# Optimization experiments

Hardware: AMD Instinct MI355X
Metric: run time of the kernel (lower is better)

Reference implementation:

```python
import jax, jax.numpy as jnp
from jax import lax
import numpy as np

T, B, D, H = 512, 256, 128, 256
SHIFT = 0.0


def setup_inputs() -> dict:
    key = jax.random.key(0)
    ks = jax.random.split(key, 11)
    s_in = 1.0 / np.sqrt(D + H)
    s_cl = 1.0 / np.sqrt(H)
    return {
        "inputs": jax.random.normal(ks[0], (T, B, D), dtype=jnp.float32),
        "Wf": jax.random.normal(ks[1], (H, D + H), dtype=jnp.float32) * s_in,
        "bf": jax.random.normal(ks[2], (H,), dtype=jnp.float32) * s_in,
        "Wi": jax.random.normal(ks[3], (H, D + H), dtype=jnp.float32) * s_in,
        "bi": jax.random.normal(ks[4], (H,), dtype=jnp.float32) * s_in,
        "Wg": jax.random.normal(ks[5], (H, D + H), dtype=jnp.float32) * s_in,
        "bg": jax.random.normal(ks[6], (H,), dtype=jnp.float32) * s_in,
        "Wo": jax.random.normal(ks[7], (H, D + H), dtype=jnp.float32) * s_in,
        "bo": jax.random.normal(ks[8], (H,), dtype=jnp.float32) * s_in,
        "Wc": jax.random.normal(ks[9], (1, H), dtype=jnp.float32) * s_cl,
        "bc": jax.random.normal(ks[10], (1,), dtype=jnp.float32) * s_cl,
    }


def reference(inputs, Wf, bf, Wi, bi, Wg, bg, Wo, bo, Wc, bc):
    # Fuse the four gate linears into one GEMM per step: [4H, D+H]
    W = jnp.concatenate([Wf, Wi, Wg, Wo], axis=0)
    b = jnp.concatenate([bf, bi, bg, bo], axis=0)
    h = W.shape[0] // 4
    batch = inputs.shape[1]

    def step(carry, x):
        hx, cx = carry
        combined = jnp.concatenate([x, hx], axis=1)      # [B, D+H]
        z = combined @ W.T + b                            # [B, 4H]
        f = jax.nn.sigmoid(z[:, 0 * h:1 * h])
        i = jax.nn.sigmoid(z[:, 1 * h:2 * h])
        g = jnp.tanh(z[:, 2 * h:3 * h])
        o = jax.nn.sigmoid(z[:, 3 * h:4 * h])
        cx = f * cx + i * g
        hx = o * jnp.tanh(cx)
        return (hx, cx), hx

    h0 = jnp.zeros((batch, h), dtype=inputs.dtype)
    c0 = jnp.zeros((batch, h), dtype=inputs.dtype)
    (hx, cx), hs = lax.scan(step, (h0, c0), inputs)       # hs: [T, B, H]

    logits = hs @ Wc.T + bc                               # [T, B, 1]
    probs = jax.nn.sigmoid(logits + SHIFT)
    return (jnp.concatenate([probs, 1.0 - probs], axis=-1), hx, cx)
```

## Files before the change

kernel.cpp:

```cpp
#include <hip/hip_runtime.h>
#include <hip/hip_bf16.h>


#define T_STEPS 512
#define BATCH   256
#define DIN     128
#define HID     256
#define KDIM    384
#define LDK     392
#define GRIDN   128
#define BLOCKT  512
#define NPOLL   96

typedef __attribute__((ext_vector_type(8))) short short8;
typedef __attribute__((ext_vector_type(4))) short short4v;
typedef __attribute__((ext_vector_type(4))) float f32x4;

__device__ __forceinline__ unsigned short f2bf(float f) {
    unsigned u = __float_as_uint(f);
    unsigned r = (u + 0x7FFFu + ((u >> 16) & 1u)) >> 16;
    return (unsigned short)r;
}
__device__ __forceinline__ float bf2f(unsigned short s) {
    return __uint_as_float(((unsigned)s) << 16);
}
__device__ __forceinline__ float sigmoid_f(float x) {
    return 1.f / (1.f + __expf(-x));
}
__device__ __forceinline__ float tanh_f(float x) {
    float e = __expf(2.f * x);
    return 1.f - 2.f / (e + 1.f);
}
__device__ __forceinline__ void poll_load2_sc0(const unsigned int* p, uint4& a,
                                               uint4& b) {
    asm volatile(
        "global_load_dwordx4 %0, %2, off sc0\n\t"
        "global_load_dwordx4 %1, %2, off offset:16 sc0\n\t"
        "s_waitcnt vmcnt(0)"
        : "=&v"(a), "=&v"(b) : "v"(p) : "memory");
}
__device__ __forceinline__ void poll_load2_sc1(const unsigned int* p, uint4& a,
                                               uint4& b) {
    asm volatile(
        "global_load_dwordx4 %0, %2, off sc1\n\t"
        "global_load_dwordx4 %1, %2, off offset:16 sc1\n\t"
        "s_waitcnt vmcnt(0)"
        : "=&v"(a), "=&v"(b) : "v"(p) : "memory");
}
__device__ __forceinline__ void store_plain_u32(unsigned int* p, unsigned int v) {
    asm volatile("global_store_dword %0, %1, off" :: "v"(p), "v"(v) : "memory");
}
__device__ __forceinline__ void store_sc1_u32(unsigned int* p, unsigned int v) {
    asm volatile("global_store_dword %0, %1, off sc1" :: "v"(p), "v"(v) : "memory");
}
__device__ __forceinline__ unsigned pack2bf(unsigned lo, unsigned hi) {
    return (hi & 0xFFFF0000u) | (lo >> 16);
}
__device__ __forceinline__ bool tags_ok2(const uint4& a, const uint4& b,
                                         unsigned tag) {
    return ((a.x ^ tag) & 0xFFFFu) == 0 && ((a.y ^ tag) & 0xFFFFu) == 0 &&
           ((a.z ^ tag) & 0xFFFFu) == 0 && ((a.w ^ tag) & 0xFFFFu) == 0 &&
           ((b.x ^ tag) & 0xFFFFu) == 0 && ((b.y ^ tag) & 0xFFFFu) == 0 &&
           ((b.z ^ tag) & 0xFFFFu) == 0 && ((b.w ^ tag) & 0xFFFFu) == 0;
}

__global__ __launch_bounds__(256) void pack_w(
    const float* __restrict__ Wf, const float* __restrict__ Wi,
    const float* __restrict__ Wg, const float* __restrict__ Wo,
    unsigned short* __restrict__ Wp) {
    int idx = blockIdx.x * 256 + threadIdx.x;
    int n = idx / KDIM;
    int k = idx - n * KDIM;
    int g = n >> 8, j = n & 255;
    const float* s = (g == 0) ? Wf : (g == 1) ? Wi : (g == 2) ? Wg : Wo;
    Wp[idx] = f2bf(s[j * KDIM + k]);
}

__global__ __launch_bounds__(256) void pack_b(
    const float* __restrict__ bf, const float* __restrict__ bi,
    const float* __restrict__ bg, const float* __restrict__ bo,
    float* __restrict__ bp) {
    int n = blockIdx.x * 256 + threadIdx.x;
    int g = n >> 8, j = n & 255;
    const float* s = (g == 0) ? bf : (g == 1) ? bi : (g == 2) ? bg : bo;
    bp[n] = s[j];
}

__global__ __launch_bounds__(256) void init_k(unsigned int* __restrict__ hxp) {
    int tid = blockIdx.x * 256 + threadIdx.x;
    hxp[tid] = 0u;
    hxp[65536 + tid] = 0u;
    hxp[131072 + tid] = 0u;
    hxp[196608 + tid] = 0u;
}

__global__ __launch_bounds__(BLOCKT, 1) void lstm_persist(
    const float* __restrict__ X,
    const unsigned short* __restrict__ W,
    const float* __restrict__ bias,
    unsigned int* __restrict__ hxp,
    unsigned short* __restrict__ hist,
    float* __restrict__ out) {
    __shared__ __align__(16) unsigned short W_s[128 * LDK];
    __shared__ __align__(16) unsigned short comb_s[16 * LDK];
    __shared__ __align__(16) float z_s[8 * 272];
    __shared__ int fastok_s;

    const int tid = threadIdx.x;
    const int bg = blockIdx.x & 15, jg = blockIdx.x >> 4;
    const int b0 = bg * 16, j0 = jg * 32;
    const int wave = tid >> 6, lane = tid & 63;
    const int l16 = lane & 15, quad = lane >> 4;
    const int bi = tid >> 5, jj = tid & 31;
    const int b = b0 + bi, j = j0 + jj;

#pragma unroll
    for (int c = 0; c < 12; ++c) {
        int q = c * 512 + tid;
        int row = q / 48, c8 = q - row * 48;
        int g = row >> 5, jr = row & 31;
        short8 v = *(const short8*)(W + ((g * 256 + j0 + jr) * KDIM + c8 * 8));
        *(short8*)(&W_s[row * LDK + c8 * 8]) = v;
    }
    const float bs0 = bias[0 * HID + j];
    const float bs1 = bias[1 * HID + j];
    const float bs2 = bias[2 * HID + j];
    const float bs3 = bias[3 * HID + j];
    if (tid == 0) fastok_s = 1;

    float c_reg = 0.f;
    float h_final = 0.f;

    const unsigned short* arow = &comb_s[l16 * LDK + quad * 8];
    const unsigned short* brow = &W_s[(wave * 16 + l16) * LDK + quad * 8];

    float4 xv = *(const float4*)(X + b * DIN + jj * 4);
    {
        short4v r;
        r.x = (short)f2bf(xv.x); r.y = (short)f2bf(xv.y);
        r.z = (short)f2bf(xv.z); r.w = (short)f2bf(xv.w);
        *(short4v*)(&comb_s[bi * LDK + jj * 4]) = r;
    }
    xv = *(const float4*)(X + (size_t)1 * BATCH * DIN + b * DIN + jj * 4);
    __syncthreads();

    f32x4 acc_x0 = {0.f, 0.f, 0.f, 0.f}, acc_x1 = {0.f, 0.f, 0.f, 0.f};
#pragma unroll
    for (int kt = 0; kt < 2; ++kt) {
        short8 a0 = *(const short8*)(arow + (2 * kt) * 32);
        short8 b0v = *(const short8*)(brow + (2 * kt) * 32);
        short8 a1 = *(const short8*)(arow + (2 * kt + 1) * 32);
        short8 b1v = *(const short8*)(brow + (2 * kt + 1) * 32);
        acc_x0 = __builtin_amdgcn_mfma_f32_16x16x32_bf16(a0, b0v, acc_x0, 0, 0, 0);
        acc_x1 = __builtin_amdgcn_mfma_f32_16x16x32_bf16(a1, b1v, acc_x1, 0, 0, 0);
    }

    for (int k = 0; k < T_STEPS; ++k) {
        const unsigned tag = (unsigned)k;
        const unsigned int* fb =
            hxp + (k & 1) * 65536 + (b0 + bi) * HID + jj * 8;
        const unsigned int* sb = fb + 131072;
        uint4 a, bq;
        const int usefast = fastok_s;

        if (usefast) {
            int tries = NPOLL;
            bool ok = false;
            for (;;) {
                poll_load2_sc0(fb, a, bq);
                if (tags_ok2(a, bq, tag)) { ok = true; break; }
                if (--tries == 0) break;
                __builtin_amdgcn_s_sleep(1);
            }
            if (!ok) {
                fastok_s = 0;
                for (;;) {
                    poll_load2_sc1(sb, a, bq);
                    if (tags_ok2(a, bq, tag)) break;
                    __builtin_amdgcn_s_sleep(1);
                }
            }
        } else {
            for (;;) {
                poll_load2_sc1(sb, a, bq);
                if (tags_ok2(a, bq, tag)) break;
                __builtin_amdgcn_s_sleep(1);
            }
        }

        {
            uint4 p0;
            p0.x = pack2bf(a.x, a.y);   p0.y = pack2bf(a.z, a.w);
            p0.z = pack2bf(bq.x, bq.y); p0.w = pack2bf(bq.z, bq.w);
            *(uint4*)(&comb_s[bi * LDK + DIN + jj * 8]) = p0;
        }
        __syncthreads();

        f32x4 acc0 = acc_x0, acc1 = acc_x1;
#pragma unroll
        for (int kt = 2; kt < 6; ++kt) {
            short8 a0 = *(const short8*)(arow + (2 * kt) * 32);
            short8 b0v = *(const short8*)(brow + (2 * kt) * 32);
            short8 a1 = *(const short8*)(arow + (2 * kt + 1) * 32);
            short8 b1v = *(const short8*)(brow + (2 * kt + 1) * 32);
            acc0 = __builtin_amdgcn_mfma_f32_16x16x32_bf16(a0, b0v, acc0, 0, 0, 0);
            acc1 = __builtin_amdgcn_mfma_f32_16x16x32_bf16(a1, b1v, acc1, 0, 0, 0);
        }
#pragma unroll
        for (int r = 0; r < 4; ++r)
            z_s[wave * 272 + (quad * 4 + r) * 17 + l16] = acc0[r] + acc1[r];
        __syncthreads();

        const int zc = bi * 17 + (jj & 15);
        const int zw = (jj >> 4) * 272;
        float zf = z_s[zw + 0 * 544 + zc] + bs0;
        float zi = z_s[zw + 1 * 544 + zc] + bs1;
        float zg = z_s[zw + 2 * 544 + zc] + bs2;
        float zo = z_s[zw + 3 * 544 + zc] + bs3;
        float fg = sigmoid_f(zf);
        float ig = sigmoid_f(zi);
        float gg = tanh_f(zg);
        float og = sigmoid_f(zo);
        c_reg = fg * c_reg + ig * gg;
        float hval = og * tanh_f(c_reg);
        unsigned short hb = f2bf(hval);
        unsigned int hword = ((unsigned)hb << 16) | (unsigned)(k + 1);
        unsigned int* fdst = hxp + ((k + 1) & 1) * 65536 + b * HID + j;
        store_plain_u32(fdst, hword);
        store_sc1_u32(fdst + 131072, hword);
        hist[(size_t)k * BATCH * HID + b * HID + j] = hb;

        if (k + 1 < T_STEPS) {
            short4v r;
            r.x = (short)f2bf(xv.x); r.y = (short)f2bf(xv.y);
            r.z = (short)f2bf(xv.z); r.w = (short)f2bf(xv.w);
            *(short4v*)(&comb_s[bi * LDK + jj * 4]) = r;
            if (k + 2 < T_STEPS) {
                xv = *(const float4*)(X + (size_t)(k + 2) * BATCH * DIN +
                                      b * DIN + jj * 4);
            }
        } else {
            h_final = hval;
        }
        __syncthreads();

        if (k + 1 < T_STEPS) {
            f32x4 ax0 = {0.f, 0.f, 0.f, 0.f}, ax1 = {0.f, 0.f, 0.f, 0.f};
#pragma unroll
            for (int kt = 0; kt < 2; ++kt) {
                short8 a0 = *(const short8*)(arow + (2 * kt) * 32);
                short8 b0v = *(const short8*)(brow + (2 * kt) * 32);
                short8 a1 = *(const short8*)(arow + (2 * kt + 1) * 32);
                short8 b1v = *(const short8*)(brow + (2 * kt + 1) * 32);
                ax0 = __builtin_amdgcn_mfma_f32_16x16x32_bf16(a0, b0v, ax0, 0, 0, 0);
                ax1 = __builtin_amdgcn_mfma_f32_16x16x32_bf16(a1, b1v, ax1, 0, 0, 0);
            }
            acc_x0 = ax0; acc_x1 = ax1;
        }
    }

    out[T_STEPS * BATCH * 2 + b * HID + j] = h_final;
    out[T_STEPS * BATCH * 2 + BATCH * HID + b * HID + j] = c_reg;
}

__global__ __launch_bounds__(256) void probs_k(
    const unsigned short* __restrict__ hist, const float* __restrict__ Wc,
    const float* __restrict__ bc, float* __restrict__ out) {
    const int wave = threadIdx.x >> 6, lane = threadIdx.x & 63;
    const size_t row = (size_t)blockIdx.x * 4 + wave;
    const unsigned short* h = hist + row * HID;
    short4v hv = *(const short4v*)(h + lane * 4);
    const float4 wv = *(const float4*)(Wc + lane * 4);
    float p = bf2f((unsigned short)hv.x) * wv.x + bf2f((unsigned short)hv.y) * wv.y +
              bf2f((unsigned short)hv.z) * wv.z + bf2f((unsigned short)hv.w) * wv.w;
#pragma unroll
    for (int off = 32; off >= 1; off >>= 1) p += __shfl_down(p, off);
    if (lane == 0) {
        float prob = 1.f / (1.f + __expf(-(p + bc[0])));
        out[row * 2]     = prob;
        out[row * 2 + 1] = 1.f - prob;
    }
}

extern "C" void kernel_launch(void* const* d_in, const int* in_sizes, int n_in,
                              void* d_out, int out_size, void* d_ws, size_t ws_size,
                              hipStream_t stream) {
    const float* X  = (const float*)d_in[0];
    const float* Wf = (const float*)d_in[1];
    const float* bfp= (const float*)d_in[2];
    const float* Wi = (const float*)d_in[3];
    const float* bip= (const float*)d_in[4];
    const float* Wg = (const float*)d_in[5];
    const float* bgp= (const float*)d_in[6];
    const float* Wo = (const float*)d_in[7];
    const float* bop= (const float*)d_in[8];
    const float* Wc = (const float*)d_in[9];
    const float* bc = (const float*)d_in[10];
    float* out = (float*)d_out;

    char* ws = (char*)d_ws;
    unsigned short* Wpack = (unsigned short*)(ws);
    float* bias = (float*)(ws + 786432);
    unsigned int* hxp = (unsigned int*)(ws + 790528);
    unsigned short* hist = (unsigned short*)(ws + 1839104);

    pack_w<<<1536, 256, 0, stream>>>(Wf, Wi, Wg, Wo, Wpack);
    pack_b<<<4, 256, 0, stream>>>(bfp, bip, bgp, bop, bias);
    init_k<<<256, 256, 0, stream>>>(hxp);

    void* kargs[6] = {(void*)&X, (void*)&Wpack, (void*)&bias,
                      (void*)&hxp, (void*)&hist, (void*)&out};
    (void)hipLaunchCooperativeKernel((const void*)lstm_persist, dim3(GRIDN),
                                     dim3(BLOCKT), kargs, 0, stream);

    probs_k<<<32768, 256, 0, stream>>>(hist, Wc, bc, out);
}
```

Measured before the change: 1.295 ms.

## Halve persistent grid, keep weights in registers, double-buffer x to drop a barrier

The persistent LSTM now runs 64 blocks of 1024 threads instead of 128 blocks of 512, so each block owns 64 hidden units. The B-operand weights move from shared memory into per-wave registers (12 short8 fragments). The bf16 x slice is double-buffered in shared memory at two offsets, which removes one __syncthreads per timestep. The fast-path poll loop also drops its s_sleep. The intent is to halve the number of cross-block pollers, cut LDS traffic and cut per-step barrier latency on the serial recurrence, at the cost of higher register pressure and twice the per-block work.

```diff
diff --git a/kernel.cpp b/kernel.cpp
--- a/kernel.cpp
+++ b/kernel.cpp
@@ -7,9 +7,9 @@
 #define DIN     128
 #define HID     256
 #define KDIM    384
-#define LDK     392
-#define GRIDN   128
-#define BLOCKT  512
+#define LDK2    520
+#define GRIDN   64
+#define BLOCKT  1024
 #define NPOLL   96
 
 typedef __attribute__((ext_vector_type(8))) short short8;
@@ -31,21 +31,17 @@
     float e = __expf(2.f * x);
     return 1.f - 2.f / (e + 1.f);
 }
-__device__ __forceinline__ void poll_load2_sc0(const unsigned int* p, uint4& a,
-                                               uint4& b) {
+__device__ __forceinline__ void poll_load1_sc0(const unsigned int* p, uint4& a) {
     asm volatile(
-        "global_load_dwordx4 %0, %2, off sc0\n\t"
-        "global_load_dwordx4 %1, %2, off offset:16 sc0\n\t"
+        "global_load_dwordx4 %0, %1, off sc0\n\t"
         "s_waitcnt vmcnt(0)"
-        : "=&v"(a), "=&v"(b) : "v"(p) : "memory");
-}
-__device__ __forceinline__ void poll_load2_sc1(const unsigned int* p, uint4& a,
-                                               uint4& b) {
+        : "=&v"(a) : "v"(p) : "memory");
+}
+__device__ __forceinline__ void poll_load1_sc1(const unsigned int* p, uint4& a) {
     asm volatile(
-        "global_load_dwordx4 %0, %2, off sc1\n\t"
-        "global_load_dwordx4 %1, %2, off offset:16 sc1\n\t"
+        "global_load_dwordx4 %0, %1, off sc1\n\t"
         "s_waitcnt vmcnt(0)"
-        : "=&v"(a), "=&v"(b) : "v"(p) : "memory");
+        : "=&v"(a) : "v"(p) : "memory");
 }
 __device__ __forceinline__ void store_plain_u32(unsigned int* p, unsigned int v) {
     asm volatile("global_store_dword %0, %1, off" :: "v"(p), "v"(v) : "memory");
@@ -56,12 +52,9 @@
 __device__ __forceinline__ unsigned pack2bf(unsigned lo, unsigned hi) {
     return (hi & 0xFFFF0000u) | (lo >> 16);
 }
-__device__ __forceinline__ bool tags_ok2(const uint4& a, const uint4& b,
-                                         unsigned tag) {
+__device__ __forceinline__ bool tags_ok1(const uint4& a, unsigned tag) {
     return ((a.x ^ tag) & 0xFFFFu) == 0 && ((a.y ^ tag) & 0xFFFFu) == 0 &&
-           ((a.z ^ tag) & 0xFFFFu) == 0 && ((a.w ^ tag) & 0xFFFFu) == 0 &&
-           ((b.x ^ tag) & 0xFFFFu) == 0 && ((b.y ^ tag) & 0xFFFFu) == 0 &&
-           ((b.z ^ tag) & 0xFFFFu) == 0 && ((b.w ^ tag) & 0xFFFFu) == 0;
+           ((a.z ^ tag) & 0xFFFFu) == 0 && ((a.w ^ tag) & 0xFFFFu) == 0;
 }
 
 __global__ __launch_bounds__(256) void pack_w(
@@ -101,27 +94,25 @@
     unsigned int* __restrict__ hxp,
     unsigned short* __restrict__ hist,
     float* __restrict__ out) {
-    __shared__ __align__(16) unsigned short W_s[128 * LDK];
-    __shared__ __align__(16) unsigned short comb_s[16 * LDK];
-    __shared__ __align__(16) float z_s[8 * 272];
+    __shared__ __align__(16) unsigned short comb_s[16 * LDK2];
+    __shared__ __align__(16) float z_s[16 * 272];
     __shared__ int fastok_s;
 
     const int tid = threadIdx.x;
     const int bg = blockIdx.x & 15, jg = blockIdx.x >> 4;
-    const int b0 = bg * 16, j0 = jg * 32;
+    const int b0 = bg * 16, j0 = jg * 64;
     const int wave = tid >> 6, lane = tid & 63;
     const int l16 = lane & 15, quad = lane >> 4;
-    const int bi = tid >> 5, jj = tid & 31;
+    const int bi = wave, jj = tid & 63;
     const int b = b0 + bi, j = j0 + jj;
 
-#pragma unroll
-    for (int c = 0; c < 12; ++c) {
-        int q = c * 512 + tid;
-        int row = q / 48, c8 = q - row * 48;
-        int g = row >> 5, jr = row & 31;
-        short8 v = *(const short8*)(W + ((g * 256 + j0 + jr) * KDIM + c8 * 8));
-        *(short8*)(&W_s[row * LDK + c8 * 8]) = v;
-    }
+    const int gw = wave >> 2, jcw = ((wave & 3) << 4) + l16;
+    const unsigned short* wrow =
+        W + (size_t)(gw * HID + j0 + jcw) * KDIM + quad * 8;
+    short8 wb[12];
+#pragma unroll
+    for (int kt = 0; kt < 12; ++kt) wb[kt] = *(const short8*)(wrow + kt * 32);
+
     const float bs0 = bias[0 * HID + j];
     const float bs1 = bias[1 * HID + j];
     const float bs2 = bias[2 * HID + j];
@@ -131,80 +122,81 @@
     float c_reg = 0.f;
     float h_final = 0.f;
 
-    const unsigned short* arow = &comb_s[l16 * LDK + quad * 8];
-    const unsigned short* brow = &W_s[(wave * 16 + l16) * LDK + quad * 8];
-
-    float4 xv = *(const float4*)(X + b * DIN + jj * 4);
+    const unsigned short* arow = &comb_s[l16 * LDK2 + quad * 8];
+    unsigned short* xrow = &comb_s[bi * LDK2];
+
+    float2 xv = *(const float2*)(X + (size_t)b * DIN + jj * 2);
     {
-        short4v r;
-        r.x = (short)f2bf(xv.x); r.y = (short)f2bf(xv.y);
-        r.z = (short)f2bf(xv.z); r.w = (short)f2bf(xv.w);
-        *(short4v*)(&comb_s[bi * LDK + jj * 4]) = r;
-    }
-    xv = *(const float4*)(X + (size_t)1 * BATCH * DIN + b * DIN + jj * 4);
+        unsigned lo = f2bf(xv.x), hi = f2bf(xv.y);
+        *(unsigned*)(&xrow[jj * 2]) = (hi << 16) | lo;
+    }
+    xv = *(const float2*)(X + (size_t)BATCH * DIN + (size_t)b * DIN + jj * 2);
     __syncthreads();
 
     f32x4 acc_x0 = {0.f, 0.f, 0.f, 0.f}, acc_x1 = {0.f, 0.f, 0.f, 0.f};
 #pragma unroll
-    for (int kt = 0; kt < 2; ++kt) {
-        short8 a0 = *(const short8*)(arow + (2 * kt) * 32);
-        short8 b0v = *(const short8*)(brow + (2 * kt) * 32);
-        short8 a1 = *(const short8*)(arow + (2 * kt + 1) * 32);
-        short8 b1v = *(const short8*)(brow + (2 * kt + 1) * 32);
-        acc_x0 = __builtin_amdgcn_mfma_f32_16x16x32_bf16(a0, b0v, acc_x0, 0, 0, 0);
-        acc_x1 = __builtin_amdgcn_mfma_f32_16x16x32_bf16(a1, b1v, acc_x1, 0, 0, 0);
+    for (int kp = 0; kp < 2; ++kp) {
+        short8 a0 = *(const short8*)(arow + (2 * kp) * 32);
+        short8 a1 = *(const short8*)(arow + (2 * kp + 1) * 32);
+        acc_x0 = __builtin_amdgcn_mfma_f32_16x16x32_bf16(a0, wb[2 * kp], acc_x0, 0, 0, 0);
+        acc_x1 = __builtin_amdgcn_mfma_f32_16x16x32_bf16(a1, wb[2 * kp + 1], acc_x1, 0, 0, 0);
     }
 
     for (int k = 0; k < T_STEPS; ++k) {
         const unsigned tag = (unsigned)k;
         const unsigned int* fb =
-            hxp + (k & 1) * 65536 + (b0 + bi) * HID + jj * 8;
+            hxp + (k & 1) * 65536 + (size_t)b * HID + jj * 4;
         const unsigned int* sb = fb + 131072;
-        uint4 a, bq;
+        uint4 aq;
         const int usefast = fastok_s;
 
         if (usefast) {
             int tries = NPOLL;
             bool ok = false;
             for (;;) {
-                poll_load2_sc0(fb, a, bq);
-                if (tags_ok2(a, bq, tag)) { ok = true; break; }
+                poll_load1_sc0(fb, aq);
+                if (tags_ok1(aq, tag)) { ok = true; break; }
                 if (--tries == 0) break;
-                __builtin_amdgcn_s_sleep(1);
             }
             if (!ok) {
                 fastok_s = 0;
                 for (;;) {
-                    poll_load2_sc1(sb, a, bq);
-                    if (tags_ok2(a, bq, tag)) break;
+                    poll_load1_sc1(sb, aq);
+                    if (tags_ok1(aq, tag)) break;
                     __builtin_amdgcn_s_sleep(1);
                 }
             }
         } else {
             for (;;) {
-                poll_load2_sc1(sb, a, bq);
-                if (tags_ok2(a, bq, tag)) break;
+                poll_load1_sc1(sb, aq);
+                if (tags_ok1(aq, tag)) break;
                 __builtin_amdgcn_s_sleep(1);
             }
         }
 
         {
-            uint4 p0;
-            p0.x = pack2bf(a.x, a.y);   p0.y = pack2bf(a.z, a.w);
-            p0.z = pack2bf(bq.x, bq.y); p0.w = pack2bf(bq.z, bq.w);
-            *(uint4*)(&comb_s[bi * LDK + DIN + jj * 8]) = p0;
+            uint2 pp;
+            pp.x = pack2bf(aq.x, aq.y);
+            pp.y = pack2bf(aq.z, aq.w);
+            *(uint2*)(&xrow[128 + jj * 4]) = pp;
+        }
+        if (k + 1 < T_STEPS) {
+            unsigned lo = f2bf(xv.x), hi = f2bf(xv.y);
+            const int xoff = ((k + 1) & 1) ? 384 : 0;
+            *(unsigned*)(&xrow[xoff + jj * 2]) = (hi << 16) | lo;
+            if (k + 2 < T_STEPS)
+                xv = *(const float2*)(X + (size_t)(k + 2) * BATCH * DIN +
+                                      (size_t)b * DIN + jj * 2);
         }
         __syncthreads();
 
         f32x4 acc0 = acc_x0, acc1 = acc_x1;
 #pragma unroll
-        for (int kt = 2; kt < 6; ++kt) {
-            short8 a0 = *(const short8*)(arow + (2 * kt) * 32);
-            short8 b0v = *(const short8*)(brow + (2 * kt) * 32);
-            short8 a1 = *(const short8*)(arow + (2 * kt + 1) * 32);
-            short8 b1v = *(const short8*)(brow + (2 * kt + 1) * 32);
-            acc0 = __builtin_amdgcn_mfma_f32_16x16x32_bf16(a0, b0v, acc0, 0, 0, 0);
-            acc1 = __builtin_amdgcn_mfma_f32_16x16x32_bf16(a1, b1v, acc1, 0, 0, 0);
+        for (int kp = 0; kp < 4; ++kp) {
+            short8 a0 = *(const short8*)(arow + (4 + 2 * kp) * 32);
+            short8 a1 = *(const short8*)(arow + (5 + 2 * kp) * 32);
+            acc0 = __builtin_amdgcn_mfma_f32_16x16x32_bf16(a0, wb[4 + 2 * kp], acc0, 0, 0, 0);
+            acc1 = __builtin_amdgcn_mfma_f32_16x16x32_bf16(a1, wb[5 + 2 * kp], acc1, 0, 0, 0);
         }
 #pragma unroll
         for (int r = 0; r < 4; ++r)
@@ -213,10 +205,10 @@
 
         const int zc = bi * 17 + (jj & 15);
         const int zw = (jj >> 4) * 272;
-        float zf = z_s[zw + 0 * 544 + zc] + bs0;
-        float zi = z_s[zw + 1 * 544 + zc] + bs1;
-        float zg = z_s[zw + 2 * 544 + zc] + bs2;
-        float zo = z_s[zw + 3 * 544 + zc] + bs3;
+        float zf = z_s[zw + 0 * 1088 + zc] + bs0;
+        float zi = z_s[zw + 1 * 1088 + zc] + bs1;
+        float zg = z_s[zw + 2 * 1088 + zc] + bs2;
+        float zo = z_s[zw + 3 * 1088 + zc] + bs3;
         float fg = sigmoid_f(zf);
         float ig = sigmoid_f(zi);
         float gg = tanh_f(zg);
@@ -225,42 +217,29 @@
         float hval = og * tanh_f(c_reg);
         unsigned short hb = f2bf(hval);
         unsigned int hword = ((unsigned)hb << 16) | (unsigned)(k + 1);
-        unsigned int* fdst = hxp + ((k + 1) & 1) * 65536 + b * HID + j;
+        unsigned int* fdst = hxp + ((k + 1) & 1) * 65536 + (size_t)b * HID + j;
         store_plain_u32(fdst, hword);
         store_sc1_u32(fdst + 131072, hword);
-        hist[(size_t)k * BATCH * HID + b * HID + j] = hb;
+        hist[(size_t)k * BATCH * HID + (size_t)b * HID + j] = hb;
 
         if (k + 1 < T_STEPS) {
-            short4v r;
-            r.x = (short)f2bf(xv.x); r.y = (short)f2bf(xv.y);
-            r.z = (short)f2bf(xv.z); r.w = (short)f2bf(xv.w);
-            *(short4v*)(&comb_s[bi * LDK + jj * 4]) = r;
-            if (k + 2 < T_STEPS) {
-                xv = *(const float4*)(X + (size_t)(k + 2) * BATCH * DIN +
-                                      b * DIN + jj * 4);
-            }
+            const int xoff = ((k + 1) & 1) ? 384 : 0;
+            f32x4 ax0 = {0.f, 0.f, 0.f, 0.f}, ax1 = {0.f, 0.f, 0.f, 0.f};
+#pragma unroll
+            for (int kp = 0; kp < 2; ++kp) {
+                short8 a0 = *(const short8*)(arow + xoff + (2 * kp) * 32);
+                short8 a1 = *(const short8*)(arow + xoff + (2 * kp + 1) * 32);
+                ax0 = __builtin_amdgcn_mfma_f32_16x16x32_bf16(a0, wb[2 * kp], ax0, 0, 0, 0);
+                ax1 = __builtin_amdgcn_mfma_f32_16x16x32_bf16(a1, wb[2 * kp + 1], ax1, 0, 0, 0);
+            }
+            acc_x0 = ax0; acc_x1 = ax1;
         } else {
             h_final = hval;
         }
-        __syncthreads();
-
-        if (k + 1 < T_STEPS) {
-            f32x4 ax0 = {0.f, 0.f, 0.f, 0.f}, ax1 = {0.f, 0.f, 0.f, 0.f};
-#pragma unroll
-            for (int kt = 0; kt < 2; ++kt) {
-                short8 a0 = *(const short8*)(arow + (2 * kt) * 32);
-                short8 b0v = *(const short8*)(brow + (2 * kt) * 32);
-                short8 a1 = *(const short8*)(arow + (2 * kt + 1) * 32);
-                short8 b1v = *(const short8*)(brow + (2 * kt + 1) * 32);
-                ax0 = __builtin_amdgcn_mfma_f32_16x16x32_bf16(a0, b0v, ax0, 0, 0, 0);
-                ax1 = __builtin_amdgcn_mfma_f32_16x16x32_bf16(a1, b1v, ax1, 0, 0, 0);
-            }
-            acc_x0 = ax0; acc_x1 = ax1;
-        }
-    }
-
-    out[T_STEPS * BATCH * 2 + b * HID + j] = h_final;
-    out[T_STEPS * BATCH * 2 + BATCH * HID + b * HID + j] = c_reg;
+    }
+
+    out[T_STEPS * BATCH * 2 + (size_t)b * HID + j] = h_final;
+    out[T_STEPS * BATCH * 2 + BATCH * HID + (size_t)b * HID + j] = c_reg;
 }
 
 __global__ __launch_bounds__(256) void probs_k(
```

Result: slower. 1.417 ms (+9.4%).
